# Optimization experiments

Measured on AMD Instinct MI355X. Metric: run time of the kernel, lower is better.

Reference implementation:

```python
import jax, jax.numpy as jnp
import numpy as np

B, TE, TD, H = 8, 512, 128, 256

def setup_inputs() -> dict:
    key = jax.random.key(0)
    k1, k2, k3, k4, k5 = jax.random.split(key, 5)
    return {
        "encoder_outputs": jax.random.normal(k1, (B, TE, H), dtype=jnp.float32),
        "decoder_outputs": jax.random.normal(k2, (B, TD, H), dtype=jnp.float32),
        "W_a": jax.random.normal(k3, (H, H), dtype=jnp.float32) * (1.0 / np.sqrt(H)),
        "U_a": jax.random.normal(k4, (H, H), dtype=jnp.float32) * (1.0 / np.sqrt(H)),
        "V_a": jax.random.normal(k5, (H, 1), dtype=jnp.float32) * (1.0 / np.sqrt(H)),
    }

def reference(encoder_outputs, decoder_outputs, W_a, U_a, V_a):
    # Bahdanau additive attention.
    enc_proj = jnp.einsum("beh,hk->bek", encoder_outputs, W_a)   # [B,TE,H]
    dec_proj = jnp.einsum("bdh,hk->bdk", decoder_outputs, U_a)   # [B,TD,H]
    # Broadcast add -> tanh -> project with V_a: [B,TD,TE]
    score = jnp.tanh(enc_proj[:, None, :, :] + dec_proj[:, :, None, :])  # [B,TD,TE,H]
    score = jnp.einsum("bdeh,h->bde", score, V_a[:, 0])          # [B,TD,TE]
    attention_weights = jax.nn.softmax(score, axis=-1)           # over encoder positions
    context = jnp.einsum("bde,beh->bdh", attention_weights, encoder_outputs)
    return (context, attention_weights)
```

## Files before the change

kernel.cpp:

```cpp
#include <hip/hip_runtime.h>
#include <hip/hip_bf16.h>

#ifndef __has_builtin
#define __has_builtin(x) 0
#endif

constexpr int B_ = 8, TE_ = 512, TD_ = 128, H_ = 256;
constexpr float TWO_LOG2E = 2.8853900817779268f;
constexpr float LOG2E = 1.4426950408889634f;

typedef float  vf2    __attribute__((ext_vector_type(2)));
typedef short  bf16x8 __attribute__((ext_vector_type(8)));
typedef float  f32x4  __attribute__((ext_vector_type(4)));

__device__ __forceinline__ float exp2_fast(float x) {
#if __has_builtin(__builtin_amdgcn_exp2f)
  return __builtin_amdgcn_exp2f(x);
#else
  return exp2f(x);
#endif
}
__device__ __forceinline__ float rcp_fast(float x) {
#if __has_builtin(__builtin_amdgcn_rcpf)
  return __builtin_amdgcn_rcpf(x);
#else
  return 1.0f / x;
#endif
}
__device__ __forceinline__ vf2 fma2(vf2 a, vf2 b, vf2 c) {
#if __has_builtin(__builtin_elementwise_fma)
  return __builtin_elementwise_fma(a, b, c);
#else
  vf2 r; r.x = __fmaf_rn(a.x, b.x, c.x); r.y = __fmaf_rn(a.y, b.y, c.y); return r;
#endif
}
__device__ __forceinline__ void bf16split(float x, unsigned short& hi, unsigned short& lo) {
  unsigned u = __float_as_uint(x);
  hi = (unsigned short)(u >> 16);
  float hif = __uint_as_float((unsigned)hi << 16);
  lo = (unsigned short)(__float_as_uint(x - hif) >> 16);
}

__global__ __launch_bounds__(256)
void proj_mfma(const float* __restrict__ enc, const float* __restrict__ dec,
               const float* __restrict__ W, const float* __restrict__ U,
               float* __restrict__ ep, float* __restrict__ dp) {
  __shared__ unsigned short Ah[32][40], Al[32][40], Bh[32][40], Bl[32][40];
  const int tid = threadIdx.x;
  const int mt = blockIdx.x;
  const int n0 = blockIdx.y * 32;
  const float* A; const float* Bm; float* C; int row0;
  if (mt < 128) { A = enc; Bm = W; C = ep; row0 = mt * 32; }
  else          { A = dec; Bm = U; C = dp; row0 = (mt - 128) * 32; }
  const int w = tid >> 6, lane = tid & 63;
  const int mw = (w & 1) * 16, nw = (w >> 1) * 16;
  const int quad = lane >> 4, l16 = lane & 15;
  const int am = tid >> 3, ak = (tid & 7) * 4;
  const int bn = tid & 31, bk = (tid >> 5) * 4;

  f32x4 acc = {0.f, 0.f, 0.f, 0.f};
  for (int k0 = 0; k0 < H_; k0 += 32) {
    float4 a4 = *(const float4*)&A[(long)(row0 + am) * H_ + k0 + ak];
    unsigned short h0, l0, h1, l1, h2, l2, h3, l3;
    bf16split(a4.x, h0, l0); bf16split(a4.y, h1, l1);
    bf16split(a4.z, h2, l2); bf16split(a4.w, h3, l3);
    *(ushort4*)&Ah[am][ak] = make_ushort4(h0, h1, h2, h3);
    *(ushort4*)&Al[am][ak] = make_ushort4(l0, l1, l2, l3);
    float b0 = Bm[(long)(k0 + bk + 0) * H_ + n0 + bn];
    float b1 = Bm[(long)(k0 + bk + 1) * H_ + n0 + bn];
    float b2 = Bm[(long)(k0 + bk + 2) * H_ + n0 + bn];
    float b3 = Bm[(long)(k0 + bk + 3) * H_ + n0 + bn];
    bf16split(b0, h0, l0); bf16split(b1, h1, l1);
    bf16split(b2, h2, l2); bf16split(b3, h3, l3);
    *(ushort4*)&Bh[bn][bk] = make_ushort4(h0, h1, h2, h3);
    *(ushort4*)&Bl[bn][bk] = make_ushort4(l0, l1, l2, l3);
    __syncthreads();
    bf16x8 ah = *(const bf16x8*)&Ah[mw + l16][quad * 8];
    bf16x8 al = *(const bf16x8*)&Al[mw + l16][quad * 8];
    bf16x8 bh = *(const bf16x8*)&Bh[nw + l16][quad * 8];
    bf16x8 bl = *(const bf16x8*)&Bl[nw + l16][quad * 8];
    acc = __builtin_amdgcn_mfma_f32_16x16x32_bf16(ah, bh, acc, 0, 0, 0);
    acc = __builtin_amdgcn_mfma_f32_16x16x32_bf16(ah, bl, acc, 0, 0, 0);
    acc = __builtin_amdgcn_mfma_f32_16x16x32_bf16(al, bh, acc, 0, 0, 0);
    __syncthreads();
  }
#pragma unroll
  for (int r = 0; r < 4; ++r)
    C[(long)(row0 + mw + quad * 4 + r) * H_ + n0 + nw + l16] =
        exp2_fast(acc[r] * TWO_LOG2E);
}

__global__ __launch_bounds__(256)
void score_kernel(const float* __restrict__ ep, const float* __restrict__ dp,
                  const float* __restrict__ v, float* __restrict__ sc) {
  __shared__ __align__(16) float eps[32][68];
  __shared__ __align__(16) float dps[16][68];
  __shared__ __align__(16) float vs[64];
  const int tid = threadIdx.x;
  const int bz = blockIdx.z;
  const int b = bz >> 1;
  const int h_lo = (bz & 1) * 128;
  const int e0 = blockIdx.x * 32;
  const int d0 = blockIdx.y * 16;
  const int e = tid & 31;
  const int dg = tid >> 5;
  vf2 acc0 = {0.f, 0.f}, acc1 = {0.f, 0.f};

  for (int h0 = h_lo; h0 < h_lo + 128; h0 += 64) {
#pragma unroll
    for (int i = 0; i < 2; ++i) {
      int idx = tid + i * 256;
      int r = idx >> 4, c = (idx & 15) << 2;
      *(float4*)&eps[r][c] = *(const float4*)&ep[(long)(b * TE_ + e0 + r) * H_ + h0 + c];
    }
    {
      int r = tid >> 4, c = (tid & 15) << 2;
      *(float4*)&dps[r][c] = *(const float4*)&dp[(long)(b * TD_ + d0 + r) * H_ + h0 + c];
    }
    if (tid < 16) {
      float4 v4 = *(const float4*)&v[h0 + tid * 4];
      float4 o; o.x = -2.f * v4.x; o.y = -2.f * v4.y; o.z = -2.f * v4.z; o.w = -2.f * v4.w;
      *(float4*)&vs[tid * 4] = o;
    }
    __syncthreads();
    const vf2 one2 = {1.f, 1.f};
#pragma unroll
    for (int hh = 0; hh < 64; hh += 4) {
      float4 evf = *(const float4*)&eps[e][hh];
      float4 vvf = *(const float4*)&vs[hh];
      float4 daf = *(const float4*)&dps[dg * 2 + 0][hh];
      float4 dbf = *(const float4*)&dps[dg * 2 + 1][hh];
      vf2 ev0 = {evf.x, evf.y}, ev1 = {evf.z, evf.w};
      vf2 vv0 = {vvf.x, vvf.y}, vv1 = {vvf.z, vvf.w};
      vf2 da0 = {daf.x, daf.y}, da1 = {daf.z, daf.w};
      vf2 db0 = {dbf.x, dbf.y}, db1 = {dbf.z, dbf.w};
      vf2 t0 = ev0 * da0 + one2;
      vf2 t1 = ev1 * da1 + one2;
      vf2 u0 = ev0 * db0 + one2;
      vf2 u1 = ev1 * db1 + one2;
      vf2 r0, r1, s0, s1;
      r0.x = rcp_fast(t0.x); r0.y = rcp_fast(t0.y);
      r1.x = rcp_fast(t1.x); r1.y = rcp_fast(t1.y);
      s0.x = rcp_fast(u0.x); s0.y = rcp_fast(u0.y);
      s1.x = rcp_fast(u1.x); s1.y = rcp_fast(u1.y);
      acc0 = fma2(vv0, r0, acc0); acc0 = fma2(vv1, r1, acc0);
      acc1 = fma2(vv0, s0, acc1); acc1 = fma2(vv1, s1, acc1);
    }
    __syncthreads();
  }
  long base = ((long)(bz & 1) * B_ * TD_ + (long)b * TD_ + d0 + dg * 2) * TE_ + e0 + e;
  sc[base] = acc0.x + acc0.y;
  sc[base + TE_] = acc1.x + acc1.y;
}

__global__ __launch_bounds__(64)
void softmax_kernel(const float* __restrict__ sc, float* __restrict__ attn) {
  const long row = blockIdx.x;
  const float* p0 = sc + row * TE_;
  const float* p1 = sc + ((long)B_ * TD_ + row) * TE_;
  float* pout = attn + row * TE_;
  const int t = threadIdx.x;
  float x[8];
  float m = -1e30f;
#pragma unroll
  for (int k = 0; k < 8; ++k) {
    x[k] = p0[t + 64 * k] + p1[t + 64 * k];
    m = fmaxf(m, x[k]);
  }
#pragma unroll
  for (int off = 32; off; off >>= 1) m = fmaxf(m, __shfl_xor(m, off, 64));
  float s = 0.f;
#pragma unroll
  for (int k = 0; k < 8; ++k) { x[k] = exp2_fast((x[k] - m) * LOG2E); s += x[k]; }
#pragma unroll
  for (int off = 32; off; off >>= 1) s += __shfl_xor(s, off, 64);
  const float r = rcp_fast(s);
#pragma unroll
  for (int k = 0; k < 8; ++k) pout[t + 64 * k] = x[k] * r;
}

__global__ __launch_bounds__(256)
void ctx_mfma(const float* __restrict__ attn, const float* __restrict__ enc,
              float* __restrict__ ctx) {
  __shared__ unsigned short Ah[32][40], Al[32][40], Bh[32][40], Bl[32][40];
  const int tid = threadIdx.x;
  const int m0 = blockIdx.x * 32;
  const int n0 = blockIdx.y * 32;
  const int b = blockIdx.z;
  const float* A = attn + (long)b * TD_ * TE_;
  const float* E = enc + (long)b * TE_ * H_;
  const int w = tid >> 6, lane = tid & 63;
  const int mw = (w & 1) * 16, nw = (w >> 1) * 16;
  const int quad = lane >> 4, l16 = lane & 15;
  const int am = tid >> 3, ak = (tid & 7) * 4;
  const int bn = tid & 31, bk = (tid >> 5) * 4;

  f32x4 acc = {0.f, 0.f, 0.f, 0.f};
  for (int k0 = 0; k0 < TE_; k0 += 32) {
    float4 a4 = *(const float4*)&A[(long)(m0 + am) * TE_ + k0 + ak];
    unsigned short h0, l0, h1, l1, h2, l2, h3, l3;
    bf16split(a4.x, h0, l0); bf16split(a4.y, h1, l1);
    bf16split(a4.z, h2, l2); bf16split(a4.w, h3, l3);
    *(ushort4*)&Ah[am][ak] = make_ushort4(h0, h1, h2, h3);
    *(ushort4*)&Al[am][ak] = make_ushort4(l0, l1, l2, l3);
    float b0 = E[(long)(k0 + bk + 0) * H_ + n0 + bn];
    float b1 = E[(long)(k0 + bk + 1) * H_ + n0 + bn];
    float b2 = E[(long)(k0 + bk + 2) * H_ + n0 + bn];
    float b3 = E[(long)(k0 + bk + 3) * H_ + n0 + bn];
    bf16split(b0, h0, l0); bf16split(b1, h1, l1);
    bf16split(b2, h2, l2); bf16split(b3, h3, l3);
    *(ushort4*)&Bh[bn][bk] = make_ushort4(h0, h1, h2, h3);
    *(ushort4*)&Bl[bn][bk] = make_ushort4(l0, l1, l2, l3);
    __syncthreads();
    bf16x8 ah = *(const bf16x8*)&Ah[mw + l16][quad * 8];
    bf16x8 al = *(const bf16x8*)&Al[mw + l16][quad * 8];
    bf16x8 bh = *(const bf16x8*)&Bh[nw + l16][quad * 8];
    bf16x8 bl = *(const bf16x8*)&Bl[nw + l16][quad * 8];
    acc = __builtin_amdgcn_mfma_f32_16x16x32_bf16(ah, bh, acc, 0, 0, 0);
    acc = __builtin_amdgcn_mfma_f32_16x16x32_bf16(ah, bl, acc, 0, 0, 0);
    acc = __builtin_amdgcn_mfma_f32_16x16x32_bf16(al, bh, acc, 0, 0, 0);
    __syncthreads();
  }
#pragma unroll
  for (int r = 0; r < 4; ++r)
    ctx[((long)b * TD_ + m0 + mw + quad * 4 + r) * H_ + n0 + nw + l16] = acc[r];
}

extern "C" void kernel_launch(void* const* d_in, const int* in_sizes, int n_in,
                              void* d_out, int out_size, void* d_ws, size_t ws_size,
                              hipStream_t stream) {
  const float* enc = (const float*)d_in[0];
  const float* dec = (const float*)d_in[1];
  const float* Wa  = (const float*)d_in[2];
  const float* Ua  = (const float*)d_in[3];
  const float* Va  = (const float*)d_in[4];

  float* out  = (float*)d_out;
  float* ctx  = out;
  float* attn = out + (long)B_ * TD_ * H_;

  float* ep = (float*)d_ws;
  float* dp = ep + (long)B_ * TE_ * H_;
  float* sc = dp + (long)B_ * TD_ * H_;

  proj_mfma<<<dim3(160, 8), 256, 0, stream>>>(enc, dec, Wa, Ua, ep, dp);
  score_kernel<<<dim3(TE_ / 32, TD_ / 16, 2 * B_), 256, 0, stream>>>(ep, dp, Va, sc);
  softmax_kernel<<<dim3(B_ * TD_), 64, 0, stream>>>(sc, attn);
  ctx_mfma<<<dim3(TD_ / 32, H_ / 32, B_), 256, 0, stream>>>(attn, enc, ctx);
}
```

Before: 99.90 us.

## Fuse softmax into context GEMM and prefetch encoder tiles

Removes the separate softmax kernel. Each context-GEMM block now loads its 32 rows of the two partial score halves, runs a row softmax in registers with 8-lane shuffles, writes the attention weights (only from the n0==0 blocks), and feeds the normalized values straight into the bf16-split MFMA loop. This drops one kernel launch and the global round trip of the attention matrix. In exchange, every column block recomputes the softmax (8x redundant score reads and exp work), and 64 float4 registers per thread are held across the loop, which may reduce occupancy. Encoder tile loads are also prefetched one iteration ahead.

```diff
diff --git a/kernel.cpp b/kernel.cpp
--- a/kernel.cpp
+++ b/kernel.cpp
@@ -153,65 +153,93 @@
   sc[base + TE_] = acc1.x + acc1.y;
 }
 
-__global__ __launch_bounds__(64)
-void softmax_kernel(const float* __restrict__ sc, float* __restrict__ attn) {
-  const long row = blockIdx.x;
-  const float* p0 = sc + row * TE_;
-  const float* p1 = sc + ((long)B_ * TD_ + row) * TE_;
-  float* pout = attn + row * TE_;
-  const int t = threadIdx.x;
-  float x[8];
-  float m = -1e30f;
-#pragma unroll
-  for (int k = 0; k < 8; ++k) {
-    x[k] = p0[t + 64 * k] + p1[t + 64 * k];
-    m = fmaxf(m, x[k]);
-  }
-#pragma unroll
-  for (int off = 32; off; off >>= 1) m = fmaxf(m, __shfl_xor(m, off, 64));
-  float s = 0.f;
-#pragma unroll
-  for (int k = 0; k < 8; ++k) { x[k] = exp2_fast((x[k] - m) * LOG2E); s += x[k]; }
-#pragma unroll
-  for (int off = 32; off; off >>= 1) s += __shfl_xor(s, off, 64);
-  const float r = rcp_fast(s);
-#pragma unroll
-  for (int k = 0; k < 8; ++k) pout[t + 64 * k] = x[k] * r;
-}
-
 __global__ __launch_bounds__(256)
-void ctx_mfma(const float* __restrict__ attn, const float* __restrict__ enc,
-              float* __restrict__ ctx) {
+void ctx_sm(const float* __restrict__ sc, const float* __restrict__ enc,
+            float* __restrict__ attn, float* __restrict__ ctx) {
   __shared__ unsigned short Ah[32][40], Al[32][40], Bh[32][40], Bl[32][40];
   const int tid = threadIdx.x;
   const int m0 = blockIdx.x * 32;
   const int n0 = blockIdx.y * 32;
   const int b = blockIdx.z;
-  const float* A = attn + (long)b * TD_ * TE_;
+  const float* s0p = sc + ((long)b * TD_ + m0) * TE_;
+  const float* s1p = sc + ((long)B_ * TD_ + (long)b * TD_ + m0) * TE_;
   const float* E = enc + (long)b * TE_ * H_;
+
   const int w = tid >> 6, lane = tid & 63;
   const int mw = (w & 1) * 16, nw = (w >> 1) * 16;
   const int quad = lane >> 4, l16 = lane & 15;
   const int am = tid >> 3, ak = (tid & 7) * 4;
   const int bn = tid & 31, bk = (tid >> 5) * 4;
 
+  float4 xv[16];
+  float mx = -1e30f;
+#pragma unroll
+  for (int k = 0; k < 16; ++k) {
+    long off = (long)am * TE_ + k * 32 + ak;
+    float4 a = *(const float4*)&s0p[off];
+    float4 c = *(const float4*)&s1p[off];
+    float4 x; x.x = a.x + c.x; x.y = a.y + c.y; x.z = a.z + c.z; x.w = a.w + c.w;
+    xv[k] = x;
+    mx = fmaxf(mx, fmaxf(fmaxf(x.x, x.y), fmaxf(x.z, x.w)));
+  }
+#pragma unroll
+  for (int off = 1; off < 8; off <<= 1) mx = fmaxf(mx, __shfl_xor(mx, off, 64));
+  float sum = 0.f;
+#pragma unroll
+  for (int k = 0; k < 16; ++k) {
+    float4 x = xv[k];
+    x.x = exp2_fast((x.x - mx) * LOG2E);
+    x.y = exp2_fast((x.y - mx) * LOG2E);
+    x.z = exp2_fast((x.z - mx) * LOG2E);
+    x.w = exp2_fast((x.w - mx) * LOG2E);
+    xv[k] = x;
+    sum += x.x + x.y + x.z + x.w;
+  }
+#pragma unroll
+  for (int off = 1; off < 8; off <<= 1) sum += __shfl_xor(sum, off, 64);
+  const float rs = rcp_fast(sum);
+
+  if (n0 == 0) {
+    float* po = attn + ((long)b * TD_ + m0 + am) * TE_;
+#pragma unroll
+    for (int k = 0; k < 16; ++k) {
+      float4 x = xv[k];
+      float4 o; o.x = x.x * rs; o.y = x.y * rs; o.z = x.z * rs; o.w = x.w * rs;
+      *(float4*)&po[k * 32 + ak] = o;
+    }
+  }
+
+  float b0, b1, b2, b3;
+  b0 = E[(long)(0 + bk + 0) * H_ + n0 + bn];
+  b1 = E[(long)(0 + bk + 1) * H_ + n0 + bn];
+  b2 = E[(long)(0 + bk + 2) * H_ + n0 + bn];
+  b3 = E[(long)(0 + bk + 3) * H_ + n0 + bn];
+
   f32x4 acc = {0.f, 0.f, 0.f, 0.f};
-  for (int k0 = 0; k0 < TE_; k0 += 32) {
-    float4 a4 = *(const float4*)&A[(long)(m0 + am) * TE_ + k0 + ak];
-    unsigned short h0, l0, h1, l1, h2, l2, h3, l3;
-    bf16split(a4.x, h0, l0); bf16split(a4.y, h1, l1);
-    bf16split(a4.z, h2, l2); bf16split(a4.w, h3, l3);
-    *(ushort4*)&Ah[am][ak] = make_ushort4(h0, h1, h2, h3);
-    *(ushort4*)&Al[am][ak] = make_ushort4(l0, l1, l2, l3);
-    float b0 = E[(long)(k0 + bk + 0) * H_ + n0 + bn];
-    float b1 = E[(long)(k0 + bk + 1) * H_ + n0 + bn];
-    float b2 = E[(long)(k0 + bk + 2) * H_ + n0 + bn];
-    float b3 = E[(long)(k0 + bk + 3) * H_ + n0 + bn];
-    bf16split(b0, h0, l0); bf16split(b1, h1, l1);
-    bf16split(b2, h2, l2); bf16split(b3, h3, l3);
-    *(ushort4*)&Bh[bn][bk] = make_ushort4(h0, h1, h2, h3);
-    *(ushort4*)&Bl[bn][bk] = make_ushort4(l0, l1, l2, l3);
-    __syncthreads();
+  for (int k = 0; k < 16; ++k) {
+    {
+      float4 x = xv[k];
+      unsigned short h0, l0, h1, l1, h2, l2, h3, l3;
+      bf16split(x.x * rs, h0, l0); bf16split(x.y * rs, h1, l1);
+      bf16split(x.z * rs, h2, l2); bf16split(x.w * rs, h3, l3);
+      *(ushort4*)&Ah[am][ak] = make_ushort4(h0, h1, h2, h3);
+      *(ushort4*)&Al[am][ak] = make_ushort4(l0, l1, l2, l3);
+    }
+    {
+      unsigned short h0, l0, h1, l1, h2, l2, h3, l3;
+      bf16split(b0, h0, l0); bf16split(b1, h1, l1);
+      bf16split(b2, h2, l2); bf16split(b3, h3, l3);
+      *(ushort4*)&Bh[bn][bk] = make_ushort4(h0, h1, h2, h3);
+      *(ushort4*)&Bl[bn][bk] = make_ushort4(l0, l1, l2, l3);
+    }
+    __syncthreads();
+    if (k < 15) {
+      int k0n = (k + 1) * 32;
+      b0 = E[(long)(k0n + bk + 0) * H_ + n0 + bn];
+      b1 = E[(long)(k0n + bk + 1) * H_ + n0 + bn];
+      b2 = E[(long)(k0n + bk + 2) * H_ + n0 + bn];
+      b3 = E[(long)(k0n + bk + 3) * H_ + n0 + bn];
+    }
     bf16x8 ah = *(const bf16x8*)&Ah[mw + l16][quad * 8];
     bf16x8 al = *(const bf16x8*)&Al[mw + l16][quad * 8];
     bf16x8 bh = *(const bf16x8*)&Bh[nw + l16][quad * 8];
@@ -245,6 +273,5 @@
 
   proj_mfma<<<dim3(160, 8), 256, 0, stream>>>(enc, dec, Wa, Ua, ep, dp);
   score_kernel<<<dim3(TE_ / 32, TD_ / 16, 2 * B_), 256, 0, stream>>>(ep, dp, Va, sc);
-  softmax_kernel<<<dim3(B_ * TD_), 64, 0, stream>>>(sc, attn);
-  ctx_mfma<<<dim3(TD_ / 32, H_ / 32, B_), 256, 0, stream>>>(attn, enc, ctx);
-}
+  ctx_sm<<<dim3(TD_ / 32, H_ / 32, B_), 256, 0, stream>>>(sc, enc, attn, ctx);
+}
```

Measured after the change: 98.49 us. About the same (-1.4%).
